# Kernel tuning notes

Measured on AMD Instinct MI355X. Metric: run time of the kernel, lower is better.

The kernel has to match this reference:

```python
import jax, jax.numpy as jnp
import numpy as np

DIM, HEADS, DIM_HEAD = 1024, 16, 64


def setup_inputs() -> dict:
    key = jax.random.key(0)
    k1, k2, k3, k4 = jax.random.split(key, 4)
    x = jax.random.normal(k1, (4, 2048, DIM), dtype=jnp.float32)
    # nn.Linear(dim, 3*dim, bias=False): weight [3*dim, dim]; y = x @ W.T
    W_qkv = jax.random.normal(k2, (3 * DIM, DIM), dtype=jnp.float32) * (DIM ** -0.5)
    W_proj = jax.random.normal(k3, (DIM, DIM), dtype=jnp.float32) * (DIM ** -0.5)
    b_proj = jax.random.normal(k4, (DIM,), dtype=jnp.float32) * 0.02
    return {"x": x, "W_qkv": W_qkv, "W_proj": W_proj, "b_proj": b_proj}


def reference(x, W_qkv, W_proj, b_proj):
    B, N, C = x.shape
    H, D = HEADS, DIM_HEAD
    scale = D ** -0.5
    qkv = x @ W_qkv.T                                   # [B, N, 3C]
    qkv = qkv.reshape(B, N, 3, H, D).transpose(2, 0, 3, 1, 4)  # [3, B, H, N, D]
    q, k, v = qkv[0], qkv[1], qkv[2]
    dots = jnp.einsum('bhid,bhjd->bhij', q, k) * scale  # [B, H, N, N]
    attn = jax.nn.softmax(dots, axis=-1)
    out = jnp.einsum('bhij,bhjd->bhid', attn, v)        # [B, H, N, D]
    out = out.transpose(0, 2, 1, 3).reshape(B, N, C)
    return out @ W_proj.T + b_proj
```

## Files before the change

kernel.cpp:

```cpp
#include <hip/hip_runtime.h>
#include <hip/hip_bf16.h>
#include <stdint.h>

typedef __bf16 bf16x4 __attribute__((ext_vector_type(4)));
typedef __bf16 bf16x8 __attribute__((ext_vector_type(8)));
typedef float  f32x4  __attribute__((ext_vector_type(4)));

#define LOG2E 1.44269504088896f

__device__ __forceinline__ void gl2lds16(const __bf16* g, __bf16* l) {
    __builtin_amdgcn_global_load_lds(
        (const __attribute__((address_space(1))) void*)g,
        (__attribute__((address_space(3))) void*)l, 16, 0, 0);
}

__global__ __launch_bounds__(256) void cvt3_f32_bf16(
    const float* __restrict__ x,  __bf16* __restrict__ xb,
    const float* __restrict__ wq, __bf16* __restrict__ wqb,
    const float* __restrict__ wp, __bf16* __restrict__ wpb) {
    const int bid = blockIdx.x;
    const float* in; __bf16* out; int base;
    if (bid < 4096)      { in = x;  out = xb;  base = bid; }
    else if (bid < 5632) { in = wq; out = wqb; base = bid - 4096; }
    else                 { in = wp; out = wpb; base = bid - 5632; }
    size_t i = ((size_t)base * 256 + threadIdx.x) * 8;
    float4 a = ((const float4*)(in + i))[0];
    float4 b = ((const float4*)(in + i))[1];
    bf16x8 v;
    v[0] = (__bf16)a.x; v[1] = (__bf16)a.y; v[2] = (__bf16)a.z; v[3] = (__bf16)a.w;
    v[4] = (__bf16)b.x; v[5] = (__bf16)b.y; v[6] = (__bf16)b.z; v[7] = (__bf16)b.w;
    *(bf16x8*)(out + i) = v;
}

template<typename TC>
__global__ __launch_bounds__(256) void gemm_bt_bf16(
    const __bf16* __restrict__ A, const __bf16* __restrict__ B,
    const float* __restrict__ bias, TC* __restrict__ C,
    int M, int N, int K, int lda, int ldb, int ldc)
{
    __shared__ __bf16 As[128][32];
    __shared__ __bf16 Bs[128][32];
    const int tid = threadIdx.x;
    const int wave = tid >> 6, lane = tid & 63;
    const int lr = lane & 15, lq = lane >> 4;
    const int m0 = blockIdx.y * 128, n0 = blockIdx.x * 128;
    const int wm = (wave >> 1) * 64, wn = (wave & 1) * 64;

    f32x4 acc[4][4] = {};

    const int sr = lane >> 2;
    const int sc = (lane & 3) * 8;
    const __bf16* ag[2]; const __bf16* bg[2];
    __bf16* alds[2]; __bf16* blds[2];
    for (int t = 0; t < 2; ++t) {
        int chunk = wave * 2 + t;
        ag[t] = A + (size_t)(m0 + chunk * 16 + sr) * lda + sc;
        bg[t] = B + (size_t)(n0 + chunk * 16 + sr) * ldb + sc;
        alds[t] = &As[0][0] + chunk * 512;
        blds[t] = &Bs[0][0] + chunk * 512;
    }

    for (int k0 = 0; k0 < K; k0 += 32) {
        __syncthreads();
        gl2lds16(ag[0] + k0, alds[0]);
        gl2lds16(ag[1] + k0, alds[1]);
        gl2lds16(bg[0] + k0, blds[0]);
        gl2lds16(bg[1] + k0, blds[1]);
        __syncthreads();
        bf16x8 af[4], bf[4];
        for (int i = 0; i < 4; ++i) af[i] = *(const bf16x8*)&As[wm + i * 16 + lr][lq * 8];
        for (int j = 0; j < 4; ++j) bf[j] = *(const bf16x8*)&Bs[wn + j * 16 + lr][lq * 8];
        for (int i = 0; i < 4; ++i)
            for (int j = 0; j < 4; ++j)
                acc[i][j] = __builtin_amdgcn_mfma_f32_16x16x32_bf16(bf[j], af[i], acc[i][j], 0, 0, 0);
    }

    float4 bv4[4] = {{0.f,0.f,0.f,0.f},{0.f,0.f,0.f,0.f},{0.f,0.f,0.f,0.f},{0.f,0.f,0.f,0.f}};
    if (bias)
        for (int j = 0; j < 4; ++j)
            bv4[j] = *(const float4*)&bias[n0 + wn + j * 16 + lq * 4];
    for (int i = 0; i < 4; ++i) {
        const int row = m0 + wm + i * 16 + lr;
        for (int j = 0; j < 4; ++j) {
            const int col = n0 + wn + j * 16 + lq * 4;
            if constexpr (sizeof(TC) == 2) {
                bf16x4 ob;
                ob[0] = (__bf16)(acc[i][j][0] + bv4[j].x);
                ob[1] = (__bf16)(acc[i][j][1] + bv4[j].y);
                ob[2] = (__bf16)(acc[i][j][2] + bv4[j].z);
                ob[3] = (__bf16)(acc[i][j][3] + bv4[j].w);
                *(bf16x4*)&C[(size_t)row * ldc + col] = ob;
            } else {
                float4 ov;
                ov.x = acc[i][j][0] + bv4[j].x;
                ov.y = acc[i][j][1] + bv4[j].y;
                ov.z = acc[i][j][2] + bv4[j].z;
                ov.w = acc[i][j][3] + bv4[j].w;
                *(float4*)&C[(size_t)row * ldc + col] = ov;
            }
        }
    }
}

__device__ __forceinline__ void stage16(const float* __restrict__ g, __bf16* l) {
    float4 a = ((const float4*)g)[0];
    float4 b = ((const float4*)g)[1];
    float4 c = ((const float4*)g)[2];
    float4 d = ((const float4*)g)[3];
    bf16x8 lo, hi;
    lo[0] = (__bf16)a.x; lo[1] = (__bf16)a.y; lo[2] = (__bf16)a.z; lo[3] = (__bf16)a.w;
    lo[4] = (__bf16)b.x; lo[5] = (__bf16)b.y; lo[6] = (__bf16)b.z; lo[7] = (__bf16)b.w;
    hi[0] = (__bf16)c.x; hi[1] = (__bf16)c.y; hi[2] = (__bf16)c.z; hi[3] = (__bf16)c.w;
    hi[4] = (__bf16)d.x; hi[5] = (__bf16)d.y; hi[6] = (__bf16)d.z; hi[7] = (__bf16)d.w;
    ((bf16x8*)l)[0] = lo;
    ((bf16x8*)l)[1] = hi;
}
__device__ __forceinline__ void stage16(const __bf16* __restrict__ g, __bf16* l) {
    ((bf16x8*)l)[0] = ((const bf16x8*)g)[0];
    ((bf16x8*)l)[1] = ((const bf16x8*)g)[1];
}

template<typename TA, typename TB, typename TC>
__global__ __launch_bounds__(256) void gemm_bt(
    const TA* __restrict__ A, const TB* __restrict__ B,
    const float* __restrict__ bias, TC* __restrict__ C,
    int M, int N, int K, int lda, int ldb, int ldc)
{
    __shared__ __bf16 As[128][40];
    __shared__ __bf16 Bs[128][40];
    const int tid = threadIdx.x;
    const int wave = tid >> 6, lane = tid & 63;
    const int lr = lane & 15, lq = lane >> 4;
    const int m0 = blockIdx.y * 128, n0 = blockIdx.x * 128;
    const int wm = (wave >> 1) * 64, wn = (wave & 1) * 64;
    const int srow = tid >> 1, scol = (tid & 1) * 16;

    f32x4 acc[4][4] = {};
    const TA* agp = A + (size_t)(m0 + srow) * lda + scol;
    const TB* bgp = B + (size_t)(n0 + srow) * ldb + scol;

    for (int k0 = 0; k0 < K; k0 += 32) {
        __syncthreads();
        stage16(agp + k0, &As[srow][scol]);
        stage16(bgp + k0, &Bs[srow][scol]);
        __syncthreads();
        bf16x8 af[4], bf[4];
        for (int i = 0; i < 4; ++i) af[i] = *(const bf16x8*)&As[wm + i * 16 + lr][lq * 8];
        for (int j = 0; j < 4; ++j) bf[j] = *(const bf16x8*)&Bs[wn + j * 16 + lr][lq * 8];
        for (int i = 0; i < 4; ++i)
            for (int j = 0; j < 4; ++j)
                acc[i][j] = __builtin_amdgcn_mfma_f32_16x16x32_bf16(bf[j], af[i], acc[i][j], 0, 0, 0);
    }

    float4 bv4[4] = {{0.f,0.f,0.f,0.f},{0.f,0.f,0.f,0.f},{0.f,0.f,0.f,0.f},{0.f,0.f,0.f,0.f}};
    if (bias)
        for (int j = 0; j < 4; ++j)
            bv4[j] = *(const float4*)&bias[n0 + wn + j * 16 + lq * 4];
    for (int i = 0; i < 4; ++i) {
        const int row = m0 + wm + i * 16 + lr;
        for (int j = 0; j < 4; ++j) {
            const int col = n0 + wn + j * 16 + lq * 4;
            if constexpr (sizeof(TC) == 2) {
                bf16x4 ob;
                ob[0] = (__bf16)(acc[i][j][0] + bv4[j].x);
                ob[1] = (__bf16)(acc[i][j][1] + bv4[j].y);
                ob[2] = (__bf16)(acc[i][j][2] + bv4[j].z);
                ob[3] = (__bf16)(acc[i][j][3] + bv4[j].w);
                *(bf16x4*)&C[(size_t)row * ldc + col] = ob;
            } else {
                float4 ov;
                ov.x = acc[i][j][0] + bv4[j].x;
                ov.y = acc[i][j][1] + bv4[j].y;
                ov.z = acc[i][j][2] + bv4[j].z;
                ov.w = acc[i][j][3] + bv4[j].w;
                *(float4*)&C[(size_t)row * ldc + col] = ov;
            }
        }
    }
}

__global__ __launch_bounds__(512, 4) void attn_kernel(__bf16* __restrict__ qkv)
{
    __shared__ __bf16 Ks[2][64][72];
    __shared__ __bf16 Vt[2][64][72];

    const int tid = threadIdx.x;
    const int wave = tid >> 6, lane = tid & 63;
    const int lr = lane & 15, lq = lane >> 4;

    const int bid = blockIdx.x;
    const int xcd = bid & 7, slot = bid >> 3;
    const int bh = xcd * 8 + (slot >> 3);
    const int qt = slot & 7;
    const int b = bh >> 4, h = bh & 15;
    const int rowbase = b * 2048;
    const int q0 = qt * 256;
    const float c1 = 0.125f * LOG2E;

    bf16x8 qf[2][2];
    for (int mt = 0; mt < 2; ++mt)
        for (int ks = 0; ks < 2; ++ks) {
            bf16x8 v = *(const bf16x8*)(qkv +
                (size_t)(rowbase + q0 + wave * 32 + mt * 16 + lr) * 3072 + h * 64 + ks * 32 + lq * 8);
            bf16x8 w;
            for (int e = 0; e < 8; ++e) w[e] = (__bf16)((float)v[e] * c1);
            qf[mt][ks] = w;
        }

    bf16x8 ones8;
    for (int e = 0; e < 8; ++e) ones8[e] = (__bf16)1.0f;

    f32x4 l_acc[2] = {};
    f32x4 o_acc[2][4] = {};

    const int tid2 = tid & 255;
    const int kr = tid2 >> 2, kc = (tid2 & 3) * 16;
    const int g0 = tid2 & 15;
    const int vj0 = g0 * 4, vd0 = (tid2 >> 4) * 4;
    const int vcol = ((g0 >> 3) * 32) + ((g0 & 3) * 8) + (((g0 >> 2) & 1) * 4);
    const __bf16* kbase = qkv + (size_t)(rowbase + kr) * 3072 + 1024 + h * 64 + kc;
    const __bf16* vbase = qkv + (size_t)(rowbase + vj0) * 3072 + 2048 + h * 64 + vd0;

    bf16x8 ka, kb;
    uint2 t0, t1, t2, t3;

    if (wave >= 4) {
        ka = ((const bf16x8*)kbase)[0];
        kb = ((const bf16x8*)kbase)[1];
        *(bf16x8*)&Ks[0][kr][kc] = ka;
        *(bf16x8*)(&Ks[0][kr][kc] + 8) = kb;
    } else {
        t0 = *(const uint2*)(vbase);
        t1 = *(const uint2*)(vbase + 3072);
        t2 = *(const uint2*)(vbase + 6144);
        t3 = *(const uint2*)(vbase + 9216);
        uint2 c0 = { (t0.x & 0xffffu) | (t1.x << 16), (t2.x & 0xffffu) | (t3.x << 16) };
        uint2 d1 = { (t0.x >> 16) | (t1.x & 0xffff0000u), (t2.x >> 16) | (t3.x & 0xffff0000u) };
        uint2 c2 = { (t0.y & 0xffffu) | (t1.y << 16), (t2.y & 0xffffu) | (t3.y << 16) };
        uint2 d3 = { (t0.y >> 16) | (t1.y & 0xffff0000u), (t2.y >> 16) | (t3.y & 0xffff0000u) };
        *(uint2*)&Vt[0][vd0 + 0][vcol] = c0;
        *(uint2*)&Vt[0][vd0 + 1][vcol] = d1;
        *(uint2*)&Vt[0][vd0 + 2][vcol] = c2;
        *(uint2*)&Vt[0][vd0 + 3][vcol] = d3;
    }

    for (int it = 0; it < 32; ++it) {
        const int cur = it & 1;
        __syncthreads();

        if (it + 1 < 32) {
            if (wave >= 4) {
                const __bf16* kg = kbase + (size_t)(it + 1) * 64 * 3072;
                ka = ((const bf16x8*)kg)[0];
                kb = ((const bf16x8*)kg)[1];
            } else {
                const __bf16* vg = vbase + (size_t)(it + 1) * 64 * 3072;
                t0 = *(const uint2*)(vg);
                t1 = *(const uint2*)(vg + 3072);
                t2 = *(const uint2*)(vg + 6144);
                t3 = *(const uint2*)(vg + 9216);
            }
        }

        for (int pi = 0; pi < 2; ++pi) {
            f32x4 s[2][2] = {};
            for (int ks = 0; ks < 2; ++ks) {
                bf16x8 kf0 = *(const bf16x8*)&Ks[cur][(2 * pi + 0) * 16 + lr][ks * 32 + lq * 8];
                bf16x8 kf1 = *(const bf16x8*)&Ks[cur][(2 * pi + 1) * 16 + lr][ks * 32 + lq * 8];
                for (int mt = 0; mt < 2; ++mt) {
                    s[mt][0] = __builtin_amdgcn_mfma_f32_16x16x32_bf16(kf0, qf[mt][ks], s[mt][0], 0, 0, 0);
                    s[mt][1] = __builtin_amdgcn_mfma_f32_16x16x32_bf16(kf1, qf[mt][ks], s[mt][1], 0, 0, 0);
                }
            }
            bf16x8 pfrag[2];
            for (int mt = 0; mt < 2; ++mt) {
                for (int t = 0; t < 2; ++t)
                    for (int r = 0; r < 4; ++r) {
                        float p = __builtin_amdgcn_exp2f(s[mt][t][r]);
                        pfrag[mt][t * 4 + r] = (__bf16)p;
                    }
            }
            for (int mt = 0; mt < 2; ++mt)
                l_acc[mt] = __builtin_amdgcn_mfma_f32_16x16x32_bf16(ones8, pfrag[mt], l_acc[mt], 0, 0, 0);
            for (int dt = 0; dt < 4; ++dt) {
                bf16x8 vf = *(const bf16x8*)&Vt[cur][dt * 16 + lr][pi * 32 + lq * 8];
                for (int mt = 0; mt < 2; ++mt)
                    o_acc[mt][dt] = __builtin_amdgcn_mfma_f32_16x16x32_bf16(vf, pfrag[mt], o_acc[mt][dt], 0, 0, 0);
            }
        }

        if (it + 1 < 32) {
            const int nb = cur ^ 1;
            if (wave >= 4) {
                *(bf16x8*)&Ks[nb][kr][kc] = ka;
                *(bf16x8*)(&Ks[nb][kr][kc] + 8) = kb;
            } else {
                uint2 c0 = { (t0.x & 0xffffu) | (t1.x << 16), (t2.x & 0xffffu) | (t3.x << 16) };
                uint2 d1 = { (t0.x >> 16) | (t1.x & 0xffff0000u), (t2.x >> 16) | (t3.x & 0xffff0000u) };
                uint2 c2 = { (t0.y & 0xffffu) | (t1.y << 16), (t2.y & 0xffffu) | (t3.y << 16) };
                uint2 d3 = { (t0.y >> 16) | (t1.y & 0xffff0000u), (t2.y >> 16) | (t3.y & 0xffff0000u) };
                *(uint2*)&Vt[nb][vd0 + 0][vcol] = c0;
                *(uint2*)&Vt[nb][vd0 + 1][vcol] = d1;
                *(uint2*)&Vt[nb][vd0 + 2][vcol] = c2;
                *(uint2*)&Vt[nb][vd0 + 3][vcol] = d3;
            }
        }
    }

    for (int mt = 0; mt < 2; ++mt) {
        float inv = 1.f / l_acc[mt][0];
        for (int dt = 0; dt < 4; ++dt) {
            bf16x4 ob;
            for (int r = 0; r < 4; ++r) ob[r] = (__bf16)(o_acc[mt][dt][r] * inv);
            *(bf16x4*)(qkv + (size_t)(rowbase + q0 + wave * 32 + mt * 16 + lr) * 3072 +
                       h * 64 + dt * 16 + lq * 4) = ob;
        }
    }
}

extern "C" void kernel_launch(void* const* d_in, const int* in_sizes, int n_in,
                              void* d_out, int out_size, void* d_ws, size_t ws_size,
                              hipStream_t stream) {
    const float* x     = (const float*)d_in[0];
    const float* Wqkv  = (const float*)d_in[1];
    const float* Wproj = (const float*)d_in[2];
    const float* bproj = (const float*)d_in[3];
    float* out   = (float*)d_out;
    __bf16* qkvb = (__bf16*)d_ws;

    const size_t QKV_E = (size_t)8192 * 3072;
    const size_t X_E   = (size_t)8192 * 1024;
    const size_t WQ_E  = (size_t)3072 * 1024;
    const size_t WP_E  = (size_t)1024 * 1024;
    const bool fast = ws_size >= (QKV_E + X_E + WQ_E + WP_E) * sizeof(__bf16);

    if (fast) {
        __bf16* xb  = qkvb + QKV_E;
        __bf16* wqb = xb + X_E;
        __bf16* wpb = wqb + WQ_E;
        cvt3_f32_bf16<<<dim3(6144), 256, 0, stream>>>(x, xb, Wqkv, wqb, Wproj, wpb);
        gemm_bt_bf16<__bf16><<<dim3(24, 64), 256, 0, stream>>>(
            xb, wqb, nullptr, qkvb, 8192, 3072, 1024, 1024, 1024, 3072);
        attn_kernel<<<dim3(512), 512, 0, stream>>>(qkvb);
        gemm_bt_bf16<float><<<dim3(8, 64), 256, 0, stream>>>(
            qkvb, wpb, bproj, out, 8192, 1024, 1024, 3072, 1024, 1024);
    } else {
        gemm_bt<float, float, __bf16><<<dim3(24, 64), 256, 0, stream>>>(
            x, Wqkv, nullptr, qkvb, 8192, 3072, 1024, 1024, 1024, 3072);
        attn_kernel<<<dim3(512), 512, 0, stream>>>(qkvb);
        gemm_bt<__bf16, float, float><<<dim3(8, 64), 256, 0, stream>>>(
            qkvb, Wproj, bproj, out, 8192, 1024, 1024, 3072, 1024, 1024);
    }
}
```

Measured before the change: 266.3 us.

## Triple-buffer LDS in bf16 GEMM to overlap global loads with MFMA

Replaces the single-buffered LDS tile loop in the bf16 GEMM with a three-stage ring buffer. Tiles are prefetched two iterations ahead via global_load_lds, and explicit vmcnt waits plus one barrier per iteration replace the two __syncthreads. This is meant to hide global memory latency behind MFMA work in both the QKV and output projection GEMMs. It triples LDS use per block, which may reduce occupancy, and it relies on hand-placed waitcnt and barrier ordering being correct.

```diff
diff --git a/kernel.cpp b/kernel.cpp
--- a/kernel.cpp
+++ b/kernel.cpp
@@ -33,13 +33,13 @@
 }
 
 template<typename TC>
-__global__ __launch_bounds__(256) void gemm_bt_bf16(
+__global__ __launch_bounds__(256) void gemm_pipe(
     const __bf16* __restrict__ A, const __bf16* __restrict__ B,
     const float* __restrict__ bias, TC* __restrict__ C,
     int M, int N, int K, int lda, int ldb, int ldc)
 {
-    __shared__ __bf16 As[128][32];
-    __shared__ __bf16 Bs[128][32];
+    __shared__ __bf16 As[3][128][32];
+    __shared__ __bf16 Bs[3][128][32];
     const int tid = threadIdx.x;
     const int wave = tid >> 6, lane = tid & 63;
     const int lr = lane & 15, lq = lane >> 4;
@@ -51,28 +51,53 @@
     const int sr = lane >> 2;
     const int sc = (lane & 3) * 8;
     const __bf16* ag[2]; const __bf16* bg[2];
-    __bf16* alds[2]; __bf16* blds[2];
+    int coff[2];
     for (int t = 0; t < 2; ++t) {
         int chunk = wave * 2 + t;
         ag[t] = A + (size_t)(m0 + chunk * 16 + sr) * lda + sc;
         bg[t] = B + (size_t)(n0 + chunk * 16 + sr) * ldb + sc;
-        alds[t] = &As[0][0] + chunk * 512;
-        blds[t] = &Bs[0][0] + chunk * 512;
-    }
-
-    for (int k0 = 0; k0 < K; k0 += 32) {
-        __syncthreads();
-        gl2lds16(ag[0] + k0, alds[0]);
-        gl2lds16(ag[1] + k0, alds[1]);
-        gl2lds16(bg[0] + k0, blds[0]);
-        gl2lds16(bg[1] + k0, blds[1]);
-        __syncthreads();
+        coff[t] = chunk * 512;
+    }
+
+    const int T = K >> 5;
+
+    auto stage = [&](int buf, int k0) {
+        gl2lds16(ag[0] + k0, &As[buf][0][0] + coff[0]);
+        gl2lds16(ag[1] + k0, &As[buf][0][0] + coff[1]);
+        gl2lds16(bg[0] + k0, &Bs[buf][0][0] + coff[0]);
+        gl2lds16(bg[1] + k0, &Bs[buf][0][0] + coff[1]);
+    };
+
+    stage(0, 0);
+    if (T > 1) {
+        stage(1, 32);
+        asm volatile("s_waitcnt vmcnt(4)" ::: "memory");
+    } else {
+        asm volatile("s_waitcnt vmcnt(0)" ::: "memory");
+    }
+    __builtin_amdgcn_s_barrier();
+
+    int ci = 0;
+    for (int t = 0; t < T; ++t) {
+        const int k0 = t << 5;
+        if (t + 2 < T) {
+            int si = ci + 2; if (si >= 3) si -= 3;
+            stage(si, k0 + 64);
+        }
+        __builtin_amdgcn_sched_barrier(0);
         bf16x8 af[4], bf[4];
-        for (int i = 0; i < 4; ++i) af[i] = *(const bf16x8*)&As[wm + i * 16 + lr][lq * 8];
-        for (int j = 0; j < 4; ++j) bf[j] = *(const bf16x8*)&Bs[wn + j * 16 + lr][lq * 8];
+        for (int i = 0; i < 4; ++i) af[i] = *(const bf16x8*)&As[ci][wm + i * 16 + lr][lq * 8];
+        for (int j = 0; j < 4; ++j) bf[j] = *(const bf16x8*)&Bs[ci][wn + j * 16 + lr][lq * 8];
         for (int i = 0; i < 4; ++i)
             for (int j = 0; j < 4; ++j)
                 acc[i][j] = __builtin_amdgcn_mfma_f32_16x16x32_bf16(bf[j], af[i], acc[i][j], 0, 0, 0);
+        __builtin_amdgcn_sched_barrier(0);
+        if (t + 2 < T)
+            asm volatile("s_waitcnt vmcnt(4)" ::: "memory");
+        else if (t + 1 < T)
+            asm volatile("s_waitcnt vmcnt(0)" ::: "memory");
+        if (t + 1 < T) __builtin_amdgcn_s_barrier();
+        ci = (ci == 2) ? 0 : ci + 1;
     }
 
     float4 bv4[4] = {{0.f,0.f,0.f,0.f},{0.f,0.f,0.f,0.f},{0.f,0.f,0.f,0.f},{0.f,0.f,0.f,0.f}};
@@ -339,10 +364,10 @@
         __bf16* wqb = xb + X_E;
         __bf16* wpb = wqb + WQ_E;
         cvt3_f32_bf16<<<dim3(6144), 256, 0, stream>>>(x, xb, Wqkv, wqb, Wproj, wpb);
-        gemm_bt_bf16<__bf16><<<dim3(24, 64), 256, 0, stream>>>(
+        gemm_pipe<__bf16><<<dim3(24, 64), 256, 0, stream>>>(
             xb, wqb, nullptr, qkvb, 8192, 3072, 1024, 1024, 1024, 3072);
         attn_kernel<<<dim3(512), 512, 0, stream>>>(qkvb);
-        gemm_bt_bf16<float><<<dim3(8, 64), 256, 0, stream>>>(
+        gemm_pipe<float><<<dim3(8, 64), 256, 0, stream>>>(
             qkvb, wpb, bproj, out, 8192, 1024, 1024, 3072, 1024, 1024);
     } else {
         gemm_bt<float, float, __bf16><<<dim3(24, 64), 256, 0, stream>>>(
```

Result: no change. 268.9 us (+1.0%).

## Replace bf16 GEMMs with 256x256 double-buffered, XOR-swizzled, phase-pipelined kernel

Applied to the files above, without the earlier changes.

Swaps the simple 128x128 single-buffered bf16 GEMM for a 512-thread 256x256-tile kernel with K-step 64. It double-buffers LDS, issues global-to-LDS loads for the next tile between four MFMA phases, and raises wave priority around the MFMA blocks. An XOR swizzle on the LDS columns is meant to avoid bank conflicts. The aim is to hide memory latency and raise data reuse per tile. The cost is fewer blocks (384 for QKV, 128 for the output projection), which may underfill the GPU, plus heavy register and LDS use.

```diff
diff --git a/kernel.cpp b/kernel.cpp
--- a/kernel.cpp
+++ b/kernel.cpp
@@ -33,39 +33,214 @@
 }
 
 template<typename TC>
-__global__ __launch_bounds__(256) void gemm_bt_bf16(
+__global__ __launch_bounds__(512, 2) void gemm_8ph(
     const __bf16* __restrict__ A, const __bf16* __restrict__ B,
     const float* __restrict__ bias, TC* __restrict__ C,
     int M, int N, int K, int lda, int ldb, int ldc)
 {
-    __shared__ __bf16 As[128][32];
-    __shared__ __bf16 Bs[128][32];
+    __shared__ __bf16 As[2][256][64];
+    __shared__ __bf16 Bs[2][256][64];
+
+    const int tid = threadIdx.x;
+    const int wave = tid >> 6, l = tid & 63;
+    const int lr = l & 15, lq = l >> 4;
+    const int wm = wave >> 2, wn = wave & 3;
+    const int m0 = blockIdx.y * 256, n0 = blockIdx.x * 256;
+
+    const int cswz = (lq * 8) ^ ((lr & 1) << 5);
+    const int cswz1 = cswz ^ 32;
+
+    const int srow = l >> 3;
+    const int selem = ((l & 7) * 8) ^ (((l >> 3) & 1) << 5);
+
+    const int rA[4] = { wm*128 + wn*16, wm*128 + wn*16 + 8,
+                        wm*128 + 64 + wn*16, wm*128 + 64 + wn*16 + 8 };
+    const int hb = wn >> 1, q = wm * 2 + (wn & 1);
+    const int rB[4] = { hb*128 + q*32, hb*128 + q*32 + 8,
+                        hb*128 + q*32 + 16, hb*128 + q*32 + 24 };
+
+    const __bf16* gA[4]; const __bf16* gB[4];
+#pragma unroll
+    for (int s = 0; s < 4; ++s) {
+        gA[s] = A + (size_t)(m0 + rA[s] + srow) * lda + selem;
+        gB[s] = B + (size_t)(n0 + rB[s] + srow) * ldb + selem;
+    }
+
+    const int T = K >> 6;
+    f32x4 acc[8][4] = {};
+
+#define STA(buf, s, kt) gl2lds16(gA[s] + ((kt) << 6), &As[buf][rA[s]][0])
+#define STB(buf, s, kt) gl2lds16(gB[s] + ((kt) << 6), &Bs[buf][rB[s]][0])
+
+    STA(0, 0, 0); STA(0, 1, 0); STA(0, 2, 0); STA(0, 3, 0);
+    STB(0, 0, 0); STB(0, 1, 0); STB(0, 2, 0); STB(0, 3, 0);
+    if (T > 1) {
+        STA(1, 0, 1); STA(1, 1, 1);
+        asm volatile("s_waitcnt vmcnt(2)" ::: "memory");
+    } else {
+        asm volatile("s_waitcnt vmcnt(0)" ::: "memory");
+    }
+    __builtin_amdgcn_s_barrier();
+
+    bf16x8 bf[4];
+    for (int t = 0; t < T; ++t) {
+        const int cur = t & 1, nxt = cur ^ 1;
+
+        {
+            bf16x8 af[4];
+#pragma unroll
+            for (int i = 0; i < 4; ++i)
+                af[i] = *(const bf16x8*)&As[cur][wm*128 + i*16 + lr][cswz];
+#pragma unroll
+            for (int j = 0; j < 4; ++j)
+                bf[j] = *(const bf16x8*)&Bs[cur][wn*64 + j*16 + lr][cswz];
+            if (t + 1 < T) { STA(nxt, 2, t + 1); STA(nxt, 3, t + 1); }
+            __builtin_amdgcn_s_barrier();
+            asm volatile("s_waitcnt lgkmcnt(0)" ::: "memory");
+            __builtin_amdgcn_s_setprio(1);
+#pragma unroll
+            for (int i = 0; i < 4; ++i)
+#pragma unroll
+                for (int j = 0; j < 4; ++j)
+                    acc[i][j] = __builtin_amdgcn_mfma_f32_16x16x32_bf16(bf[j], af[i], acc[i][j], 0, 0, 0);
+            __builtin_amdgcn_s_setprio(0);
+            __builtin_amdgcn_s_barrier();
+        }
+        {
+            bf16x8 af[4];
+#pragma unroll
+            for (int i = 0; i < 4; ++i)
+                af[i] = *(const bf16x8*)&As[cur][wm*128 + 64 + i*16 + lr][cswz];
+            if (t + 1 < T) { STB(nxt, 0, t + 1); STB(nxt, 1, t + 1); }
+            __builtin_amdgcn_s_barrier();
+            asm volatile("s_waitcnt lgkmcnt(0)" ::: "memory");
+            __builtin_amdgcn_s_setprio(1);
+#pragma unroll
+            for (int i = 0; i < 4; ++i)
+#pragma unroll
+                for (int j = 0; j < 4; ++j)
+                    acc[4 + i][j] = __builtin_amdgcn_mfma_f32_16x16x32_bf16(bf[j], af[i], acc[4 + i][j], 0, 0, 0);
+            __builtin_amdgcn_s_setprio(0);
+            __builtin_amdgcn_s_barrier();
+        }
+        {
+            bf16x8 af[4];
+#pragma unroll
+            for (int i = 0; i < 4; ++i)
+                af[i] = *(const bf16x8*)&As[cur][wm*128 + i*16 + lr][cswz1];
+#pragma unroll
+            for (int j = 0; j < 4; ++j)
+                bf[j] = *(const bf16x8*)&Bs[cur][wn*64 + j*16 + lr][cswz1];
+            if (t + 1 < T) { STB(nxt, 2, t + 1); STB(nxt, 3, t + 1); }
+            __builtin_amdgcn_s_barrier();
+            asm volatile("s_waitcnt lgkmcnt(0)" ::: "memory");
+            __builtin_amdgcn_s_setprio(1);
+#pragma unroll
+            for (int i = 0; i < 4; ++i)
+#pragma unroll
+                for (int j = 0; j < 4; ++j)
+                    acc[i][j] = __builtin_amdgcn_mfma_f32_16x16x32_bf16(bf[j], af[i], acc[i][j], 0, 0, 0);
+            __builtin_amdgcn_s_setprio(0);
+            __builtin_amdgcn_s_barrier();
+        }
+        {
+            bf16x8 af[4];
+#pragma unroll
+            for (int i = 0; i < 4; ++i)
+                af[i] = *(const bf16x8*)&As[cur][wm*128 + 64 + i*16 + lr][cswz1];
+            if (t + 2 < T) { STA(cur, 0, t + 2); STA(cur, 1, t + 2); }
+            __builtin_amdgcn_s_barrier();
+            asm volatile("s_waitcnt lgkmcnt(0)" ::: "memory");
+            __builtin_amdgcn_s_setprio(1);
+#pragma unroll
+            for (int i = 0; i < 4; ++i)
+#pragma unroll
+                for (int j = 0; j < 4; ++j)
+                    acc[4 + i][j] = __builtin_amdgcn_mfma_f32_16x16x32_bf16(bf[j], af[i], acc[4 + i][j], 0, 0, 0);
+            __builtin_amdgcn_s_setprio(0);
+            if (t + 2 < T) {
+                asm volatile("s_waitcnt vmcnt(2)" ::: "memory");
+                __builtin_amdgcn_s_barrier();
+            } else if (t + 1 < T) {
+                asm volatile("s_waitcnt vmcnt(0)" ::: "memory");
+                __builtin_amdgcn_s_barrier();
+            }
+        }
+    }
+#undef STA
+#undef STB
+
+    float4 bv4[4] = {{0.f,0.f,0.f,0.f},{0.f,0.f,0.f,0.f},{0.f,0.f,0.f,0.f},{0.f,0.f,0.f,0.f}};
+    if (bias)
+#pragma unroll
+        for (int j = 0; j < 4; ++j)
+            bv4[j] = *(const float4*)&bias[n0 + wn*64 + j*16 + lq*4];
+#pragma unroll
+    for (int ii = 0; ii < 8; ++ii) {
+        const int row = m0 + wm*128 + ii*16 + lr;
+#pragma unroll
+        for (int j = 0; j < 4; ++j) {
+            const int col = n0 + wn*64 + j*16 + lq*4;
+            if constexpr (sizeof(TC) == 2) {
+                bf16x4 ob;
+                ob[0] = (__bf16)(acc[ii][j][0] + bv4[j].x);
+                ob[1] = (__bf16)(acc[ii][j][1] + bv4[j].y);
+                ob[2] = (__bf16)(acc[ii][j][2] + bv4[j].z);
+                ob[3] = (__bf16)(acc[ii][j][3] + bv4[j].w);
+                *(bf16x4*)&C[(size_t)row * ldc + col] = ob;
+            } else {
+                float4 ov;
+                ov.x = acc[ii][j][0] + bv4[j].x;
+                ov.y = acc[ii][j][1] + bv4[j].y;
+                ov.z = acc[ii][j][2] + bv4[j].z;
+                ov.w = acc[ii][j][3] + bv4[j].w;
+                *(float4*)&C[(size_t)row * ldc + col] = ov;
+            }
+        }
+    }
+}
+
+__device__ __forceinline__ void stage16(const float* __restrict__ g, __bf16* l) {
+    float4 a = ((const float4*)g)[0];
+    float4 b = ((const float4*)g)[1];
+    float4 c = ((const float4*)g)[2];
+    float4 d = ((const float4*)g)[3];
+    bf16x8 lo, hi;
+    lo[0] = (__bf16)a.x; lo[1] = (__bf16)a.y; lo[2] = (__bf16)a.z; lo[3] = (__bf16)a.w;
+    lo[4] = (__bf16)b.x; lo[5] = (__bf16)b.y; lo[6] = (__bf16)b.z; lo[7] = (__bf16)b.w;
+    hi[0] = (__bf16)c.x; hi[1] = (__bf16)c.y; hi[2] = (__bf16)c.z; hi[3] = (__bf16)c.w;
+    hi[4] = (__bf16)d.x; hi[5] = (__bf16)d.y; hi[6] = (__bf16)d.z; hi[7] = (__bf16)d.w;
+    ((bf16x8*)l)[0] = lo;
+    ((bf16x8*)l)[1] = hi;
+}
+__device__ __forceinline__ void stage16(const __bf16* __restrict__ g, __bf16* l) {
+    ((bf16x8*)l)[0] = ((const bf16x8*)g)[0];
+    ((bf16x8*)l)[1] = ((const bf16x8*)g)[1];
+}
+
+template<typename TA, typename TB, typename TC>
+__global__ __launch_bounds__(256) void gemm_bt(
+    const TA* __restrict__ A, const TB* __restrict__ B,
+    const float* __restrict__ bias, TC* __restrict__ C,
+    int M, int N, int K, int lda, int ldb, int ldc)
+{
+    __shared__ __bf16 As[128][40];
+    __shared__ __bf16 Bs[128][40];
     const int tid = threadIdx.x;
     const int wave = tid >> 6, lane = tid & 63;
     const int lr = lane & 15, lq = lane >> 4;
     const int m0 = blockIdx.y * 128, n0 = blockIdx.x * 128;
     const int wm = (wave >> 1) * 64, wn = (wave & 1) * 64;
+    const int srow = tid >> 1, scol = (tid & 1) * 16;
 
     f32x4 acc[4][4] = {};
-
-    const int sr = lane >> 2;
-    const int sc = (lane & 3) * 8;
-    const __bf16* ag[2]; const __bf16* bg[2];
-    __bf16* alds[2]; __bf16* blds[2];
-    for (int t = 0; t < 2; ++t) {
-        int chunk = wave * 2 + t;
-        ag[t] = A + (size_t)(m0 + chunk * 16 + sr) * lda + sc;
-        bg[t] = B + (size_t)(n0 + chunk * 16 + sr) * ldb + sc;
-        alds[t] = &As[0][0] + chunk * 512;
-        blds[t] = &Bs[0][0] + chunk * 512;
-    }
+    const TA* agp = A + (size_t)(m0 + srow) * lda + scol;
+    const TB* bgp = B + (size_t)(n0 + srow) * ldb + scol;
 
     for (int k0 = 0; k0 < K; k0 += 32) {
         __syncthreads();
-        gl2lds16(ag[0] + k0, alds[0]);
-        gl2lds16(ag[1] + k0, alds[1]);
-        gl2lds16(bg[0] + k0, blds[0]);
-        gl2lds16(bg[1] + k0, blds[1]);
+        stage16(agp + k0, &As[srow][scol]);
+        stage16(bgp + k0, &Bs[srow][scol]);
         __syncthreads();
         bf16x8 af[4], bf[4];
         for (int i = 0; i < 4; ++i) af[i] = *(const bf16x8*)&As[wm + i * 16 + lr][lq * 8];
@@ -102,83 +277,6 @@
     }
 }
 
-__device__ __forceinline__ void stage16(const float* __restrict__ g, __bf16* l) {
-    float4 a = ((const float4*)g)[0];
-    float4 b = ((const float4*)g)[1];
-    float4 c = ((const float4*)g)[2];
-    float4 d = ((const float4*)g)[3];
-    bf16x8 lo, hi;
-    lo[0] = (__bf16)a.x; lo[1] = (__bf16)a.y; lo[2] = (__bf16)a.z; lo[3] = (__bf16)a.w;
-    lo[4] = (__bf16)b.x; lo[5] = (__bf16)b.y; lo[6] = (__bf16)b.z; lo[7] = (__bf16)b.w;
-    hi[0] = (__bf16)c.x; hi[1] = (__bf16)c.y; hi[2] = (__bf16)c.z; hi[3] = (__bf16)c.w;
-    hi[4] = (__bf16)d.x; hi[5] = (__bf16)d.y; hi[6] = (__bf16)d.z; hi[7] = (__bf16)d.w;
-    ((bf16x8*)l)[0] = lo;
-    ((bf16x8*)l)[1] = hi;
-}
-__device__ __forceinline__ void stage16(const __bf16* __restrict__ g, __bf16* l) {
-    ((bf16x8*)l)[0] = ((const bf16x8*)g)[0];
-    ((bf16x8*)l)[1] = ((const bf16x8*)g)[1];
-}
-
-template<typename TA, typename TB, typename TC>
-__global__ __launch_bounds__(256) void gemm_bt(
-    const TA* __restrict__ A, const TB* __restrict__ B,
-    const float* __restrict__ bias, TC* __restrict__ C,
-    int M, int N, int K, int lda, int ldb, int ldc)
-{
-    __shared__ __bf16 As[128][40];
-    __shared__ __bf16 Bs[128][40];
-    const int tid = threadIdx.x;
-    const int wave = tid >> 6, lane = tid & 63;
-    const int lr = lane & 15, lq = lane >> 4;
-    const int m0 = blockIdx.y * 128, n0 = blockIdx.x * 128;
-    const int wm = (wave >> 1) * 64, wn = (wave & 1) * 64;
-    const int srow = tid >> 1, scol = (tid & 1) * 16;
-
-    f32x4 acc[4][4] = {};
-    const TA* agp = A + (size_t)(m0 + srow) * lda + scol;
-    const TB* bgp = B + (size_t)(n0 + srow) * ldb + scol;
-
-    for (int k0 = 0; k0 < K; k0 += 32) {
-        __syncthreads();
-        stage16(agp + k0, &As[srow][scol]);
-        stage16(bgp + k0, &Bs[srow][scol]);
-        __syncthreads();
-        bf16x8 af[4], bf[4];
-        for (int i = 0; i < 4; ++i) af[i] = *(const bf16x8*)&As[wm + i * 16 + lr][lq * 8];
-        for (int j = 0; j < 4; ++j) bf[j] = *(const bf16x8*)&Bs[wn + j * 16 + lr][lq * 8];
-        for (int i = 0; i < 4; ++i)
-            for (int j = 0; j < 4; ++j)
-                acc[i][j] = __builtin_amdgcn_mfma_f32_16x16x32_bf16(bf[j], af[i], acc[i][j], 0, 0, 0);
-    }
-
-    float4 bv4[4] = {{0.f,0.f,0.f,0.f},{0.f,0.f,0.f,0.f},{0.f,0.f,0.f,0.f},{0.f,0.f,0.f,0.f}};
-    if (bias)
-        for (int j = 0; j < 4; ++j)
-            bv4[j] = *(const float4*)&bias[n0 + wn + j * 16 + lq * 4];
-    for (int i = 0; i < 4; ++i) {
-        const int row = m0 + wm + i * 16 + lr;
-        for (int j = 0; j < 4; ++j) {
-            const int col = n0 + wn + j * 16 + lq * 4;
-            if constexpr (sizeof(TC) == 2) {
-                bf16x4 ob;
-                ob[0] = (__bf16)(acc[i][j][0] + bv4[j].x);
-                ob[1] = (__bf16)(acc[i][j][1] + bv4[j].y);
-                ob[2] = (__bf16)(acc[i][j][2] + bv4[j].z);
-                ob[3] = (__bf16)(acc[i][j][3] + bv4[j].w);
-                *(bf16x4*)&C[(size_t)row * ldc + col] = ob;
-            } else {
-                float4 ov;
-                ov.x = acc[i][j][0] + bv4[j].x;
-                ov.y = acc[i][j][1] + bv4[j].y;
-                ov.z = acc[i][j][2] + bv4[j].z;
-                ov.w = acc[i][j][3] + bv4[j].w;
-                *(float4*)&C[(size_t)row * ldc + col] = ov;
-            }
-        }
-    }
-}
-
 __global__ __launch_bounds__(512, 4) void attn_kernel(__bf16* __restrict__ qkv)
 {
     __shared__ __bf16 Ks[2][64][72];
@@ -339,10 +437,10 @@
         __bf16* wqb = xb + X_E;
         __bf16* wpb = wqb + WQ_E;
         cvt3_f32_bf16<<<dim3(6144), 256, 0, stream>>>(x, xb, Wqkv, wqb, Wproj, wpb);
-        gemm_bt_bf16<__bf16><<<dim3(24, 64), 256, 0, stream>>>(
+        gemm_8ph<__bf16><<<dim3(12, 32), 512, 0, stream>>>(
             xb, wqb, nullptr, qkvb, 8192, 3072, 1024, 1024, 1024, 3072);
         attn_kernel<<<dim3(512), 512, 0, stream>>>(qkvb);
-        gemm_bt_bf16<float><<<dim3(8, 64), 256, 0, stream>>>(
+        gemm_8ph<float><<<dim3(4, 32), 512, 0, stream>>>(
             qkvb, wpb, bproj, out, 8192, 1024, 1024, 3072, 1024, 1024);
     } else {
         gemm_bt<float, float, __bf16><<<dim3(24, 64), 256, 0, stream>>>(
```

Measured after the change: 298.4 us. 1.12x slower.
